# Kernel tuning notes

Measured on AMD Instinct MI355X. Metric: run time of the kernel, lower is better.

Reference implementation:

```python
import jax, jax.numpy as jnp
import numpy as np

B, N, R, DIM = 4, 1024, 5, 1024
H, DH = 16, 64
ALPHA = 128.0
# FLAGS.fix_attention=True, a_sim=False: q * (dim_head**-0.5 * alpha**-1) * mult**-0.5
SCALE = (DH ** -0.5) * (1.0 / ALPHA) * (R ** -0.5)
EPS = 1e-5


def layernorm(x, g):
    mean = jnp.mean(x, axis=-1, keepdims=True)
    var = jnp.mean((x - mean) ** 2, axis=-1, keepdims=True)  # unbiased=False
    return (x - mean) * jax.lax.rsqrt(var + EPS) * g


def setup_inputs() -> dict:
    key = jax.random.key(0)
    ks = jax.random.split(key, 8)
    x = jax.random.normal(ks[0], (B, N, R, DIM), dtype=jnp.float32)
    mask = jax.random.bernoulli(ks[1], 0.9, (B, N))
    g_in = jnp.ones((DIM,), dtype=jnp.float32)
    Wq = jax.random.normal(ks[2], (DIM, H * DH), dtype=jnp.float32) * 0.02
    Wkv = jax.random.normal(ks[3], (DIM, 2 * DH), dtype=jnp.float32) * 0.02
    null_kv = jax.random.normal(ks[4], (2, DH), dtype=jnp.float32)
    Wout = jax.random.normal(ks[5], (H * DH, DIM), dtype=jnp.float32) * 0.02
    g_out = jnp.ones((DIM,), dtype=jnp.float32)
    return {"x": x, "mask": mask, "g_in": g_in, "Wq": Wq, "Wkv": Wkv,
            "null_kv": null_kv, "Wout": Wout, "g_out": g_out}


def reference(x, mask, g_in, Wq, Wkv, null_kv, Wout, g_out):
    # context defaults to the UN-normalized x (set before norm in the original)
    context = x
    xn = layernorm(x, g_in)                               # [b,n,r,dim]
    q = jnp.einsum('bnrc,ce->bnre', xn, Wq)               # [b,n,r,h*d]
    q = q.reshape(B, N, R, H, DH).transpose(0, 3, 1, 2, 4)  # b h n r d
    q = q * SCALE
    kv = jnp.einsum('bnrc,ce->bnre', context, Wkv)        # [b,n,r,2d] (multi-query: 1 kv head)
    k, v = kv[..., :DH], kv[..., DH:]                     # [b,n,r,d]
    # null kv token prepended along the j (sequence) axis, repeated over r
    nk = jnp.broadcast_to(null_kv[0], (B, 1, R, DH))
    nv = jnp.broadcast_to(null_kv[1], (B, 1, R, DH))
    k = jnp.concatenate([nk, k], axis=1)                  # [b,n+1,r,d]
    v = jnp.concatenate([nv, v], axis=1)
    sim = jnp.einsum('bhird,bjrd->bhij', q, k)            # [b,h,n,n+1]
    big = jnp.finfo(sim.dtype).max
    maskp = jnp.pad(mask, ((0, 0), (1, 0)), constant_values=True)  # null token always visible
    sim = jnp.where(maskp[:, None, None, :], sim, -big)
    # pb-relax: subtract detached row max, rescale by alpha
    sim = sim - jax.lax.stop_gradient(jnp.max(sim, axis=-1, keepdims=True))
    attn = jax.nn.softmax(sim * ALPHA, axis=-1)
    out = jnp.einsum('bhij,bjrd->bhird', attn, v)         # b h n r d
    out = out.transpose(0, 2, 3, 1, 4).reshape(B, N, R, H * DH)
    out = jnp.einsum('bnre,eo->bnro', out, Wout)
    return layernorm(out, g_out)
```

## Files before the change

kernel.cpp:

```cpp
#include <hip/hip_runtime.h>

#define B_   4
#define N_   1024
#define R_   5
#define DIM_ 1024
#define H_   16
#define DH_  64
#define NJ   1056
#define CDIM 320
#define MROWS (B_*N_*R_)

typedef unsigned int u32;
typedef unsigned short u16;
typedef __attribute__((ext_vector_type(8))) short bf16x8;
typedef __attribute__((ext_vector_type(4))) float f32x4;
typedef __attribute__((ext_vector_type(16))) float f32x16;

constexpr float SCALEA_ = (float)(0.05590169943749474 * 1.4426950408889634);

__device__ __forceinline__ u16 f2bf(float f) {
  u32 u = __builtin_bit_cast(u32, f);
  u32 r = (u + 0x7fffu + ((u >> 16) & 1u)) >> 16;
  return (u16)r;
}
__device__ __forceinline__ u32 pack2(float lo, float hi) {
  return (u32)f2bf(lo) | ((u32)f2bf(hi) << 16);
}
__device__ __forceinline__ void gld_lds16(void* lds, const void* g) {
  __builtin_amdgcn_global_load_lds((const __attribute__((address_space(1))) u32*)g,
                                   (__attribute__((address_space(3))) u32*)lds, 16, 0, 0);
}

__global__ __launch_bounds__(256) void prep_ln(const void* __restrict__ mask, const float* __restrict__ nullkv,
                                               const float* __restrict__ Wq, const float* __restrict__ Wkv,
                                               const float* __restrict__ Wout,
                                               const float* __restrict__ x, const float* __restrict__ gin,
                                               float* __restrict__ biasg, u16* __restrict__ kg,
                                               u16* __restrict__ vTg, u16* __restrict__ WqT,
                                               u16* __restrict__ WkvT, u16* __restrict__ WoutT,
                                               u16* __restrict__ xn, u16* __restrict__ xb) {
  const int bid = blockIdx.x, t = threadIdx.x;
  __shared__ int sfl;
  __shared__ float tile[32][33];
  __shared__ float red[8];
  if (bid >= 2353) {
    const size_t row = bid - 2353;
    const int w = t >> 6, lane = t & 63;
    const float* xr = x + row * 1024;
    f32x4 v = *(const f32x4*)(xr + t * 4);
    float s = v[0] + v[1] + v[2] + v[3];
    #pragma unroll
    for (int o = 1; o < 64; o <<= 1) s += __shfl_xor(s, o);
    if (lane == 0) red[w] = s;
    __syncthreads();
    float mean = (red[0] + red[1] + red[2] + red[3]) * (1.0f / 1024.0f);
    f32x4 d;
    float ss = 0.f;
    #pragma unroll
    for (int e = 0; e < 4; ++e) { d[e] = v[e] - mean; ss += d[e] * d[e]; }
    #pragma unroll
    for (int o = 1; o < 64; o <<= 1) ss += __shfl_xor(ss, o);
    if (lane == 0) red[4 + w] = ss;
    __syncthreads();
    float var = (red[4] + red[5] + red[6] + red[7]) * (1.0f / 1024.0f);
    float rs = rsqrtf(var + 1e-5f);
    f32x4 gv = *(const f32x4*)(gin + t * 4);
    uint2 o1, o2;
    o1.x = pack2(d[0] * rs * gv[0], d[1] * rs * gv[1]);
    o1.y = pack2(d[2] * rs * gv[2], d[3] * rs * gv[3]);
    o2.x = pack2(v[0], v[1]);
    o2.y = pack2(v[2], v[3]);
    *(uint2*)(xn + row * 1024 + t * 4) = o1;
    *(uint2*)(xb + row * 1024 + t * 4) = o2;
  } else if (bid < 17) {
    if (t == 0) sfl = 0;
    __syncthreads();
    int fl = 0;
    const u32* mw = (const u32*)mask;
    for (int i = t; i < 1024; i += 256) {
      u32 wv = mw[i];
      if (wv == 0x3f800000u) fl |= 4;
      else if (wv > 1u) fl |= 2;
      if ((i & 1) && wv == 1u) fl |= 1;
    }
    if (fl) atomicOr(&sfl, fl);
    __syncthreads();
    int fb = sfl;
    int idx = bid * 256 + t;
    if (idx < B_ * NJ) {
      int b = idx / NJ, j = idx % NJ;
      int mv;
      if (j == 0) mv = 1;
      else if (j > N_) mv = 0;
      else {
        int mode = (fb & 4) ? 2 : ((fb & 2) ? 1 : ((fb & 1) ? 0 : 3));
        int mi = b * N_ + (j - 1);
        if (mode == 0)      mv = ((const int*)mask)[mi] != 0;
        else if (mode == 1) mv = ((const unsigned char*)mask)[mi] != 0;
        else if (mode == 2) mv = ((const float*)mask)[mi] != 0.0f;
        else                mv = ((const int*)mask)[mi * 2] != 0;
      }
      biasg[idx] = mv ? 0.0f : -__builtin_inff();
    }
  } else if (bid < 177) {
    int idx = (bid - 17) * 256 + t;
    if (idx < B_ * 32 * CDIM) {
      int c  = idx % CDIM;
      int jj = (idx / CDIM) & 31;
      int b  = idx / (CDIM * 32);
      int j  = (jj == 0) ? 0 : (1024 + jj);
      u16 kvv, vvv;
      if (jj == 0) { kvv = f2bf(nullkv[c & 63]); vvv = f2bf(nullkv[64 + (c & 63)]); }
      else         { kvv = 0; vvv = 0; }
      kg [(size_t)(b * NJ + j) * CDIM + c] = kvv;
      vTg[(((size_t)b * 33 + (j >> 5)) * CDIM + c) * 32 + (j & 31)] = vvv;
    }
  } else {
    const float* W; u16* WT; int Nn, id;
    if (bid < 1201)      { W = Wq;   WT = WqT;   Nn = 1024; id = bid - 177; }
    else if (bid < 1329) { W = Wkv;  WT = WkvT;  Nn = 128;  id = bid - 1201; }
    else                 { W = Wout; WT = WoutT; Nn = 1024; id = bid - 1329; }
    const int K = 1024;
    int nb = (Nn == 128) ? 4 : 32;
    int n0 = (id % nb) * 32, k0 = (id / nb) * 32;
    int tx = t & 31, ty = t >> 5;
    #pragma unroll
    for (int e = 0; e < 4; ++e)
      tile[ty + e * 8][tx] = W[(size_t)(k0 + ty + e * 8) * Nn + n0 + tx];
    __syncthreads();
    #pragma unroll
    for (int e = 0; e < 4; ++e)
      WT[(size_t)(n0 + ty + e * 8) * K + k0 + tx] = f2bf(tile[tx][ty + e * 8]);
  }
}

__global__ __launch_bounds__(256) void ln_out(const u16* __restrict__ yb, const float* __restrict__ gout,
                                              float* __restrict__ out) {
  const size_t row = blockIdx.x;
  const int t = threadIdx.x, w = t >> 6, lane = t & 63;
  uint2 raw = *(const uint2*)(yb + row * 1024 + t * 4);
  f32x4 v;
  v[0] = __builtin_bit_cast(float, (raw.x & 0xffffu) << 16);
  v[1] = __builtin_bit_cast(float, (raw.x & 0xffff0000u));
  v[2] = __builtin_bit_cast(float, (raw.y & 0xffffu) << 16);
  v[3] = __builtin_bit_cast(float, (raw.y & 0xffff0000u));
  float s = v[0] + v[1] + v[2] + v[3];
  #pragma unroll
  for (int o = 1; o < 64; o <<= 1) s += __shfl_xor(s, o);
  __shared__ float red[8];
  if (lane == 0) red[w] = s;
  __syncthreads();
  float mean = (red[0] + red[1] + red[2] + red[3]) * (1.0f / 1024.0f);
  f32x4 d;
  float ss = 0.f;
  #pragma unroll
  for (int e = 0; e < 4; ++e) { d[e] = v[e] - mean; ss += d[e] * d[e]; }
  #pragma unroll
  for (int o = 1; o < 64; o <<= 1) ss += __shfl_xor(ss, o);
  if (lane == 0) red[4 + w] = ss;
  __syncthreads();
  float var = (red[4] + red[5] + red[6] + red[7]) * (1.0f / 1024.0f);
  float rs = rsqrtf(var + 1e-5f);
  f32x4 gv = *(const f32x4*)(gout + t * 4);
  f32x4 o;
  #pragma unroll
  for (int e = 0; e < 4; ++e) o[e] = d[e] * rs * gv[e];
  *(f32x4*)(out + row * 1024 + t * 4) = o;
}

template <int EPI>
__device__ __forceinline__ void gemm_body(const u16* __restrict__ A, const u16* __restrict__ BT,
                                          u16* __restrict__ C0, u16* __restrict__ C1,
                                          const int K, const size_t m0, const size_t n0,
                                          u16* Al , u16* Bl) {
  const int t = threadIdx.x, w = t >> 6, lane = t & 63;
  const int g = lane >> 4, i16 = lane & 15;
  const int wr = w >> 1, wc = w & 1;
  const size_t K2 = (size_t)K * 2;

  const char* asrc[2];
  const char* bsrc[2];
  #pragma unroll
  for (int s = 0; s < 2; ++s) {
    int r = (s * 4 + w) * 16 + (lane >> 2);
    int sw = (((lane & 3) ^ ((lane >> 2) & 3)) << 4);
    asrc[s] = (const char*)(A + m0 * K) + (size_t)r * K2 + sw;
    bsrc[s] = (const char*)(BT + n0 * K) + (size_t)r * K2 + sw;
  }

  f32x4 acc[4][4];
  #pragma unroll
  for (int mi = 0; mi < 4; ++mi)
    #pragma unroll
    for (int ni = 0; ni < 4; ++ni) acc[mi][ni] = (f32x4){0.f, 0.f, 0.f, 0.f};

  auto stage = [&](int kt) {
    const int slot = kt % 3;
    const size_t kb = (size_t)kt * 64;
    #pragma unroll
    for (int s = 0; s < 2; ++s) {
      gld_lds16(&Al[slot * 4096 + (s * 4 + w) * 512], asrc[s] + kb);
      gld_lds16(&Bl[slot * 4096 + (s * 4 + w) * 512], bsrc[s] + kb);
    }
  };

  stage(0);
  stage(1);
  const int NT = K >> 5;
  const int rdsw = ((g ^ (i16 & 3)) << 4);

  for (int kt = 0; kt < NT; ++kt) {
    if (kt < NT - 1) asm volatile("s_waitcnt vmcnt(4)" ::: "memory");
    else             asm volatile("s_waitcnt vmcnt(0)" ::: "memory");
    __builtin_amdgcn_s_barrier();
    __builtin_amdgcn_sched_barrier(0);

    if (kt + 2 < NT) stage(kt + 2);

    const int slot = kt % 3;
    const char* apb = (const char*)&Al[slot * 4096] + (wr * 64 + i16) * 64 + rdsw;
    const char* bpb = (const char*)&Bl[slot * 4096] + (wc * 64 + i16) * 64 + rdsw;
    bf16x8 af[4], bfr[4];
    #pragma unroll
    for (int mi = 0; mi < 4; ++mi) af[mi]  = *(const bf16x8*)(apb + mi * 1024);
    #pragma unroll
    for (int ni = 0; ni < 4; ++ni) bfr[ni] = *(const bf16x8*)(bpb + ni * 1024);
    __builtin_amdgcn_s_setprio(1);
    #pragma unroll
    for (int mi = 0; mi < 4; ++mi)
      #pragma unroll
      for (int ni = 0; ni < 4; ++ni)
        acc[mi][ni] = __builtin_amdgcn_mfma_f32_16x16x32_bf16(af[mi], bfr[ni], acc[mi][ni], 0, 0, 0);
    __builtin_amdgcn_s_setprio(0);
  }

  #pragma unroll
  for (int mi = 0; mi < 4; ++mi)
    #pragma unroll
    for (int ni = 0; ni < 4; ++ni)
      #pragma unroll
      for (int reg = 0; reg < 4; ++reg) {
        size_t gr = m0 + wr * 64 + mi * 16 + g * 4 + reg;
        int gc = (int)n0 + wc * 64 + ni * 16 + i16;
        float v = acc[mi][ni][reg];
        if (EPI == 0) {
          C0[gr * 1024 + gc] = f2bf(v * SCALEA_);
        } else if (EPI == 1) {
          int grr = (int)gr;
          int b = grr / (N_ * R_);
          int rem = grr - b * (N_ * R_);
          int n = rem / R_;
          int r = rem - n * R_;
          int j = n + 1;
          u16 val = f2bf(v);
          if (gc < DH_) C0[(size_t)(b * NJ + j) * CDIM + r * 64 + gc] = val;
          else C1[(((size_t)b * 33 + (j >> 5)) * CDIM + r * 64 + (gc - DH_)) * 32 + (j & 31)] = val;
        } else {
          C0[gr * 1024 + gc] = f2bf(v);
        }
      }
}

__global__ __launch_bounds__(256, 3) void proj(const u16* __restrict__ xn, const u16* __restrict__ WqT,
                                               u16* __restrict__ qb, const u16* __restrict__ xb,
                                               const u16* __restrict__ WkvT, u16* __restrict__ kg,
                                               u16* __restrict__ vTg) {
  __shared__ __align__(16) u16 Al[3 * 4096];
  __shared__ __align__(16) u16 Bl[3 * 4096];
  const int bid = blockIdx.x;
  const int wg = (bid & 7) * 180 + (bid >> 3);
  const int xi = wg % 9;
  const size_t m0 = (size_t)(wg / 9) * 128;
  if (xi < 8) gemm_body<0>(xn, WqT, qb, nullptr, 1024, m0, (size_t)xi * 128, Al, Bl);
  else        gemm_body<1>(xb, WkvT, kg, vTg, 1024, m0, 0, Al, Bl);
}

__global__ __launch_bounds__(256, 3) void outproj(const u16* __restrict__ attout,
                                                  const u16* __restrict__ WoutT, u16* __restrict__ yb) {
  __shared__ __align__(16) u16 Al[3 * 4096];
  __shared__ __align__(16) u16 Bl[3 * 4096];
  const int bid = blockIdx.x;
  const int wg = (bid & 7) * 160 + (bid >> 3);
  const size_t n0 = (size_t)(wg & 7) * 128;
  const size_t m0 = (size_t)(wg >> 3) * 128;
  gemm_body<2>(attout, WoutT, yb, nullptr, 1024, m0, n0, Al, Bl);
}

__global__ __launch_bounds__(256, 2) void attn_kernel(const u16* __restrict__ qb, const u16* __restrict__ kg,
                                                      const u16* __restrict__ vTg, const float* __restrict__ biasg,
                                                      u16* __restrict__ attout) {
  const int blk0 = blockIdx.x;
  const int blk = (blk0 & 7) * 128 + (blk0 >> 3);
  const int ch = blk & 1;
  const int it = (blk >> 1) & 7;
  const int h  = (blk >> 4) & 15;
  const int b  = blk >> 8;
  const int t = threadIdx.x;
  const int w = t >> 6, lane = t & 63;
  const int l31 = lane & 31, lh = lane >> 5;
  const int i0 = it * 128 + w * 32;

  __shared__ __align__(16) char Kl[2][20480];
  __shared__ __align__(16) char Vl[2][10240];

  int ksrc[5];
  #pragma unroll
  for (int s = 0; s < 5; ++s) {
    int d = w * 320 + s * 64 + lane;
    int j = d / 40, c16 = d - j * 40;
    int fj = (j & 7) ^ (j >> 3);
    ksrc[s] = j * 640 + ((c16 ^ fj) << 4);
  }
  int vsrc[3];
  #pragma unroll
  for (int s = 0; s < 3; ++s) {
    int d = s * 256 + t;
    int vc = d >> 2, sl = d & 3;
    int gv = (vc & 3) ^ ((vc >> 3) & 3);
    vsrc[s] = (ch * 160 + vc) * 64 + ((sl ^ gv) << 4);
  }
  const char* ktile = (const char*)(kg + (size_t)b * NJ * CDIM);
  const char* vtile = (const char*)(vTg + (size_t)b * 33 * CDIM * 32);

  bf16x8 qf[20];
  {
    const u16* qrow = qb + ((size_t)(b * N_ + i0 + l31) * R_) * 1024 + h * 64 + lh * 8;
    #pragma unroll
    for (int kk = 0; kk < 20; ++kk) {
      int k16 = kk * 16;
      qf[kk] = *(const bf16x8*)(qrow + (k16 >> 6) * 1024 + (k16 & 63));
    }
  }

  const float* bptr = biasg + b * NJ + lh * 4;

  f32x16 O[5];
  #pragma unroll
  for (int cf = 0; cf < 5; ++cf)
    #pragma unroll
    for (int r = 0; r < 16; ++r) O[cf][r] = 0.f;
  float d_run = 0.f;

  #pragma unroll
  for (int s = 0; s < 5; ++s)
    gld_lds16(&Kl[0][w * 5120 + s * 1024], ktile + ksrc[s]);
  {
    gld_lds16(&Vl[0][w * 1024],        vtile + vsrc[0]);
    gld_lds16(&Vl[0][4096 + w * 1024], vtile + vsrc[1]);
    if (w < 2) gld_lds16(&Vl[0][8192 + w * 1024], vtile + vsrc[2]);
  }

  const int swzK = ((l31 & 7) ^ (l31 >> 3)) << 4;
  const int swzV = ((l31 & 3) ^ ((l31 >> 3) & 3)) << 4;

  for (int jt = 0; jt < 33; ++jt) {
    const int cur = jt & 1;

    asm volatile("s_waitcnt vmcnt(0)" ::: "memory");
    __builtin_amdgcn_s_barrier();
    __builtin_amdgcn_sched_barrier(0);

    if (jt < 32) {
      const char* kt1 = ktile + (size_t)(jt + 1) * 20480;
      const char* vt1 = vtile + (size_t)(jt + 1) * 20480;
      #pragma unroll
      for (int s = 0; s < 5; ++s)
        gld_lds16(&Kl[cur ^ 1][w * 5120 + s * 1024], kt1 + ksrc[s]);
      gld_lds16(&Vl[cur ^ 1][w * 1024],        vt1 + vsrc[0]);
      gld_lds16(&Vl[cur ^ 1][4096 + w * 1024], vt1 + vsrc[1]);
      if (w < 2) gld_lds16(&Vl[cur ^ 1][8192 + w * 1024], vt1 + vsrc[2]);
    }

    const char* Kb  = &Kl[cur][0] + l31 * 640;
    const char* kb0 = Kb + ((0x00 | (lh << 4)) ^ swzK);
    const char* kb1 = Kb + ((0x20 | (lh << 4)) ^ swzK);
    const char* kb2 = Kb + ((0x40 | (lh << 4)) ^ swzK);
    const char* kb3 = Kb + ((0x60 | (lh << 4)) ^ swzK);
    f32x16 S0, S1;
    #pragma unroll
    for (int r = 0; r < 16; ++r) { S0[r] = 0.f; S1[r] = 0.f; }
    __builtin_amdgcn_s_setprio(1);
    #pragma unroll
    for (int kk = 0; kk < 20; ++kk) {
      const char* kb = ((kk & 3) == 0) ? kb0 : ((kk & 3) == 1) ? kb1 : ((kk & 3) == 2) ? kb2 : kb3;
      bf16x8 kf = *(const bf16x8*)(kb + (kk >> 2) * 128);
      if (kk & 1) S1 = __builtin_amdgcn_mfma_f32_32x32x16_bf16(kf, qf[kk], S1, 0, 0, 0);
      else        S0 = __builtin_amdgcn_mfma_f32_32x32x16_bf16(kf, qf[kk], S0, 0, 0, 0);
    }
    __builtin_amdgcn_s_setprio(0);

    f32x4 bb0 = *(const f32x4*)(bptr + (size_t)jt * 32 + 0);
    f32x4 bb1 = *(const f32x4*)(bptr + (size_t)jt * 32 + 8);
    f32x4 bb2 = *(const f32x4*)(bptr + (size_t)jt * 32 + 16);
    f32x4 bb3 = *(const f32x4*)(bptr + (size_t)jt * 32 + 24);
    float p[16];
    float ts = 0.f;
    #pragma unroll
    for (int r = 0; r < 16; ++r) {
      float bv = (r < 4) ? bb0[r & 3] : (r < 8) ? bb1[r & 3] : (r < 12) ? bb2[r & 3] : bb3[r & 3];
      float L = fminf(S0[r] + S1[r] + bv, 80.0f);
      p[r] = exp2f(L);
      ts += p[r];
    }
    d_run += ts;

    u32 pk0, pk1, pk2, pk3, pk4, pk5, pk6, pk7;
    asm("v_cvt_pk_bf16_f32 %0, %1, %2" : "=v"(pk0) : "v"(p[0]),  "v"(p[1]));
    asm("v_cvt_pk_bf16_f32 %0, %1, %2" : "=v"(pk1) : "v"(p[2]),  "v"(p[3]));
    asm("v_cvt_pk_bf16_f32 %0, %1, %2" : "=v"(pk2) : "v"(p[4]),  "v"(p[5]));
    asm("v_cvt_pk_bf16_f32 %0, %1, %2" : "=v"(pk3) : "v"(p[6]),  "v"(p[7]));
    asm("v_cvt_pk_bf16_f32 %0, %1, %2" : "=v"(pk4) : "v"(p[8]),  "v"(p[9]));
    asm("v_cvt_pk_bf16_f32 %0, %1, %2" : "=v"(pk5) : "v"(p[10]), "v"(p[11]));
    asm("v_cvt_pk_bf16_f32 %0, %1, %2" : "=v"(pk6) : "v"(p[12]), "v"(p[13]));
    asm("v_cvt_pk_bf16_f32 %0, %1, %2" : "=v"(pk7) : "v"(p[14]), "v"(p[15]));
    asm volatile("v_permlane32_swap_b32 %0, %1" : "+v"(pk0), "+v"(pk2));
    asm volatile("v_permlane32_swap_b32 %0, %1" : "+v"(pk1), "+v"(pk3));
    asm volatile("v_permlane32_swap_b32 %0, %1" : "+v"(pk4), "+v"(pk6));
    asm volatile("v_permlane32_swap_b32 %0, %1" : "+v"(pk5), "+v"(pk7));
    union { u32 u[4]; bf16x8 v; } f1, f2;
    f1.u[0] = pk0; f1.u[1] = pk1; f1.u[2] = pk2; f1.u[3] = pk3;
    f2.u[0] = pk4; f2.u[1] = pk5; f2.u[2] = pk6; f2.u[3] = pk7;

    const char* Vb  = &Vl[cur][0] + l31 * 64;
    const char* vb1 = Vb + ((lh << 4) ^ swzV);
    const char* vb2 = Vb + (((lh ^ 2) << 4) ^ swzV);
    __builtin_amdgcn_s_setprio(1);
    #pragma unroll
    for (int cf = 0; cf < 5; ++cf) {
      bf16x8 v0 = *(const bf16x8*)(vb1 + cf * 2048);
      bf16x8 v1 = *(const bf16x8*)(vb2 + cf * 2048);
      O[cf] = __builtin_amdgcn_mfma_f32_32x32x16_bf16(f1.v, v0, O[cf], 0, 0, 0);
      O[cf] = __builtin_amdgcn_mfma_f32_32x32x16_bf16(f2.v, v1, O[cf], 0, 0, 0);
    }
    __builtin_amdgcn_s_setprio(0);
  }

  d_run += __shfl_xor(d_run, 32);
  float inv = 1.0f / d_run;
  float invr[16];
  #pragma unroll
  for (int r = 0; r < 16; ++r) invr[r] = __shfl(inv, (r & 3) + 8 * (r >> 2) + 4 * lh);

  #pragma unroll
  for (int r = 0; r < 16; ++r) {
    int gi = i0 + (r & 3) + 8 * (r >> 2) + 4 * lh;
    u16* orow = attout + ((size_t)(b * N_ + gi) * R_) * 1024 + h * 64;
    #pragma unroll
    for (int cf = 0; cf < 5; ++cf) {
      int c = ch * 160 + cf * 32 + l31;
      orow[(c >> 6) * 1024 + (c & 63)] = f2bf(O[cf][r] * invr[r]);
    }
  }
}

extern "C" void kernel_launch(void* const* d_in, const int* in_sizes, int n_in,
                              void* d_out, int out_size, void* d_ws, size_t ws_size,
                              hipStream_t stream) {
  (void)in_sizes; (void)n_in; (void)out_size; (void)ws_size;
  const float* x      = (const float*)d_in[0];
  const void*  mask   = d_in[1];
  const float* g_in   = (const float*)d_in[2];
  const float* Wq     = (const float*)d_in[3];
  const float* Wkv    = (const float*)d_in[4];
  const float* nullkv = (const float*)d_in[5];
  const float* Wout   = (const float*)d_in[6];
  const float* g_out  = (const float*)d_in[7];
  float* out = (float*)d_out;

  char* base = (char*)d_ws;
  size_t off = 0;
  auto carve = [&](size_t bytes) { char* r = base + off; off += (bytes + 255) & ~(size_t)255; return r; };
  float* biasg = (float*)carve((size_t)B_ * NJ * 4);
  u16* WqT   = (u16*)carve((size_t)1024 * 1024 * 2);
  u16* WkvT  = (u16*)carve((size_t)128 * 1024 * 2);
  u16* WoutT = (u16*)carve((size_t)1024 * 1024 * 2);
  u16* xn    = (u16*)carve((size_t)MROWS * 1024 * 2);
  u16* xb    = (u16*)carve((size_t)MROWS * 1024 * 2);
  u16* qb    = (u16*)carve((size_t)MROWS * 1024 * 2);
  u16* kg    = (u16*)carve((size_t)B_ * NJ * CDIM * 2);
  u16* vTg   = (u16*)carve((size_t)B_ * 33 * CDIM * 32 * 2);
  u16* attout = xn;
  u16* yb     = xb;

  prep_ln<<<2353 + MROWS, 256, 0, stream>>>(mask, nullkv, Wq, Wkv, Wout, x, g_in,
                                            biasg, kg, vTg, WqT, WkvT, WoutT, xn, xb);
  proj<<<1440, 256, 0, stream>>>(xn, WqT, qb, xb, WkvT, kg, vTg);
  attn_kernel<<<1024, 256, 0, stream>>>(qb, kg, vTg, biasg, attout);
  outproj<<<1280, 256, 0, stream>>>(attout, WoutT, yb);
  ln_out<<<MROWS, 256, 0, stream>>>(yb, g_out, out);
}
```

Measured before the change: 364.4 us.

## Triple-buffer K tiles with two-ahead prefetch and single-buffer V loaded per tile

K tiles in the attention kernel move to a three-slot LDS ring and are prefetched two tiles ahead. V now uses a single LDS buffer that is loaded at the start of each iteration and waited on with partial vmcnt waits plus a second barrier before the PV MFMAs. The aim is to hide K load latency more deeply while keeping total LDS use moderate. In exchange it adds a second block-wide barrier per tile, and V load latency now only overlaps with the QK and softmax work of the same tile. LDS per block also grows, which could press on two-blocks-per-CU occupancy.

Measured after the change: 366.7 us. Within noise of the previous version (+0.6%).

```diff
diff --git a/kernel.cpp b/kernel.cpp
--- a/kernel.cpp
+++ b/kernel.cpp
@@ -300,8 +300,8 @@
   const int l31 = lane & 31, lh = lane >> 5;
   const int i0 = it * 128 + w * 32;
 
-  __shared__ __align__(16) char Kl[2][20480];
-  __shared__ __align__(16) char Vl[2][10240];
+  __shared__ __align__(16) char Kl[3][20480];
+  __shared__ __align__(16) char Vl[10240];
 
   int ksrc[5];
   #pragma unroll
@@ -344,34 +344,35 @@
   #pragma unroll
   for (int s = 0; s < 5; ++s)
     gld_lds16(&Kl[0][w * 5120 + s * 1024], ktile + ksrc[s]);
-  {
-    gld_lds16(&Vl[0][w * 1024],        vtile + vsrc[0]);
-    gld_lds16(&Vl[0][4096 + w * 1024], vtile + vsrc[1]);
-    if (w < 2) gld_lds16(&Vl[0][8192 + w * 1024], vtile + vsrc[2]);
-  }
+  #pragma unroll
+  for (int s = 0; s < 5; ++s)
+    gld_lds16(&Kl[1][w * 5120 + s * 1024], ktile + 20480 + ksrc[s]);
 
   const int swzK = ((l31 & 7) ^ (l31 >> 3)) << 4;
   const int swzV = ((l31 & 3) ^ ((l31 >> 3) & 3)) << 4;
 
   for (int jt = 0; jt < 33; ++jt) {
-    const int cur = jt & 1;
-
-    asm volatile("s_waitcnt vmcnt(0)" ::: "memory");
+    const int slot = jt % 3;
+
+    if (jt < 32) asm volatile("s_waitcnt vmcnt(5)" ::: "memory");
+    else         asm volatile("s_waitcnt vmcnt(0)" ::: "memory");
     __builtin_amdgcn_s_barrier();
     __builtin_amdgcn_sched_barrier(0);
 
-    if (jt < 32) {
-      const char* kt1 = ktile + (size_t)(jt + 1) * 20480;
-      const char* vt1 = vtile + (size_t)(jt + 1) * 20480;
+    {
+      const char* vt = vtile + (size_t)jt * 20480;
+      gld_lds16(&Vl[w * 1024],        vt + vsrc[0]);
+      gld_lds16(&Vl[4096 + w * 1024], vt + vsrc[1]);
+      if (w < 2) gld_lds16(&Vl[8192 + w * 1024], vt + vsrc[2]);
+    }
+    if (jt + 2 < 33) {
+      const char* kt2 = ktile + (size_t)(jt + 2) * 20480;
       #pragma unroll
       for (int s = 0; s < 5; ++s)
-        gld_lds16(&Kl[cur ^ 1][w * 5120 + s * 1024], kt1 + ksrc[s]);
-      gld_lds16(&Vl[cur ^ 1][w * 1024],        vt1 + vsrc[0]);
-      gld_lds16(&Vl[cur ^ 1][4096 + w * 1024], vt1 + vsrc[1]);
-      if (w < 2) gld_lds16(&Vl[cur ^ 1][8192 + w * 1024], vt1 + vsrc[2]);
-    }
-
-    const char* Kb  = &Kl[cur][0] + l31 * 640;
+        gld_lds16(&Kl[(jt + 2) % 3][w * 5120 + s * 1024], kt2 + ksrc[s]);
+    }
+
+    const char* Kb  = &Kl[slot][0] + l31 * 640;
     const char* kb0 = Kb + ((0x00 | (lh << 4)) ^ swzK);
     const char* kb1 = Kb + ((0x20 | (lh << 4)) ^ swzK);
     const char* kb2 = Kb + ((0x40 | (lh << 4)) ^ swzK);
@@ -421,7 +422,12 @@
     f1.u[0] = pk0; f1.u[1] = pk1; f1.u[2] = pk2; f1.u[3] = pk3;
     f2.u[0] = pk4; f2.u[1] = pk5; f2.u[2] = pk6; f2.u[3] = pk7;
 
-    const char* Vb  = &Vl[cur][0] + l31 * 64;
+    if (jt <= 30) asm volatile("s_waitcnt vmcnt(5)" ::: "memory");
+    else          asm volatile("s_waitcnt vmcnt(0)" ::: "memory");
+    __builtin_amdgcn_s_barrier();
+    __builtin_amdgcn_sched_barrier(0);
+
+    const char* Vb  = &Vl[0] + l31 * 64;
     const char* vb1 = Vb + ((lh << 4) ^ swzV);
     const char* vb2 = Vb + (((lh ^ 2) << 4) ^ swzV);
     __builtin_amdgcn_s_setprio(1);
```
